# Optimization experiments

Hardware: AMD Instinct MI355X
Metric: run time of the kernel (lower is better)

Reference implementation:

```python
import jax, jax.numpy as jnp
import numpy as np

N_NODES = 100000
N_EDGES = 1600000
IN_F = 128
HEADS = 4
D_K = 32
OUT_TOTAL = HEADS * D_K


def setup_inputs() -> dict:
    key = jax.random.key(0)
    k1, k2, k3, k4, k5, k6 = jax.random.split(key, 6)
    x = jax.random.normal(k1, (N_NODES, IN_F), dtype=jnp.float32)
    edge_index = jax.random.randint(k2, (2, N_EDGES), 0, N_NODES, dtype=jnp.int64)
    # torch nn.Linear weights: [out, in], xavier-uniform init
    def xavier(k, shape):
        fan_out, fan_in = shape
        lim = float(np.sqrt(6.0 / (fan_in + fan_out)))
        return jax.random.uniform(k, shape, dtype=jnp.float32, minval=-lim, maxval=lim)
    Wq = xavier(k3, (OUT_TOTAL, IN_F))
    Wk = xavier(k4, (OUT_TOTAL, IN_F))
    Wv = xavier(k5, (OUT_TOTAL, IN_F))
    # D init_type='uniform': U(-1, 1)
    D = jax.random.uniform(k6, (HEADS, D_K), dtype=jnp.float32, minval=-1.0, maxval=1.0)
    return {"x": x, "Wq": Wq, "Wk": Wk, "Wv": Wv, "D": D, "edge_index": edge_index}


def reference(x, Wq, Wk, Wv, D, edge_index):
    N = x.shape[0]
    scale = 1.0 / np.sqrt(D_K)
    Q = (x @ Wq.T).reshape(N, HEADS, D_K)
    K = (x @ Wk.T).reshape(N, HEADS, D_K)
    V = (x @ Wv.T).reshape(N, HEADS, D_K)
    row, col = edge_index[0], edge_index[1]
    K_i = K[row]              # [E, H, d]
    Q_j = Q[col]              # [E, H, d]
    diff = K_i - Q_j
    # non-self edges: diff^T diag(D) diff ; self edges: K^T diag(D) Q
    score_edge = jnp.sum(diff * D * diff, axis=-1)          # [E, H]
    score_self = jnp.sum(K_i * D * Q[row], axis=-1)         # [E, H]
    self_mask = (row == col)[:, None]
    scores = jnp.where(self_mask, score_self, score_edge)
    scores = jax.nn.leaky_relu(scores * scale, 0.2)
    # segment softmax over destination node `row`
    smax = jax.ops.segment_max(scores, row, num_segments=N)  # [N, H]
    ex = jnp.exp(scores - smax[row])
    ssum = jax.ops.segment_sum(ex, row, num_segments=N)      # [N, H]
    alpha = ex / (ssum[row] + 1e-16)
    # scatter-add aggregate alpha * V[col] into destination rows
    out = jax.ops.segment_sum(alpha[:, :, None] * V[col], row, num_segments=N)
    return out.reshape(N, OUT_TOTAL)
```

## Files before the change

kernel.cpp:

```cpp
#include <hip/hip_runtime.h>
#include <hip/hip_fp16.h>
#include <cmath>


#define HEADS 4
#define DK 32
#define FDIM 128
#define BINSHIFT 8
#define BINCAP 6144

typedef _Float16 f16x8 __attribute__((ext_vector_type(8)));
typedef float f32x4 __attribute__((ext_vector_type(4)));

__global__ __launch_bounds__(256) void split_w(
    const float* __restrict__ Wq, const float* __restrict__ Wk,
    const float* __restrict__ Wv, _Float16* __restrict__ Whf,
    _Float16* __restrict__ Wlf, int* __restrict__ bin_cursor, int nb)
{
    const int gid = blockIdx.x * 256 + threadIdx.x;
    if (gid < nb) bin_cursor[gid] = 0;

    const int p = blockIdx.x;
    const float* __restrict__ W = (p == 0) ? Wq : (p == 1 ? Wk : Wv);
#pragma unroll
    for (int i = 0; i < 8; ++i) {
        const int id = i * 256 + threadIdx.x;
        const int g  = id >> 8;
        const int kc = (id >> 6) & 3;
        const int l  = id & 63;
        const int row  = g * 16 + (l & 15);
        const int col0 = kc * 32 + (l >> 4) * 8;
        const float* src = W + row * FDIM + col0;
        const float4 v0 = *reinterpret_cast<const float4*>(src);
        const float4 v1 = *reinterpret_cast<const float4*>(src + 4);
        const float vv[8] = {v0.x, v0.y, v0.z, v0.w, v1.x, v1.y, v1.z, v1.w};
        f16x8 h, lo;
#pragma unroll
        for (int j = 0; j < 8; ++j) {
            _Float16 hh = (_Float16)vv[j];
            h[j]  = hh;
            lo[j] = (_Float16)(vv[j] - (float)hh);
        }
        const size_t off = ((size_t)((p * 8 + g) * 4 + kc) * 64 + l) * 8;
        *reinterpret_cast<f16x8*>(Whf + off) = h;
        *reinterpret_cast<f16x8*>(Wlf + off) = lo;
    }
}

__device__ __forceinline__ int swz_idx(int row, int kk) {
    return (row * FDIM + kk) ^ ((row & 7) << 3);
}

__device__ __forceinline__ void stage_x(
    const float* __restrict__ src, _Float16* __restrict__ dh,
    _Float16* __restrict__ dl, int n0, int nmax, int tid)
{
    const int kk0 = (tid & 15) * 8;
    const int r0  = tid >> 4;
#pragma unroll
    for (int i = 0; i < 4; ++i) {
        const int row = i * 16 + r0;
        float4 v0 = make_float4(0.f, 0.f, 0.f, 0.f), v1 = v0;
        if (n0 + row < nmax) {
            const float* p = src + (size_t)(n0 + row) * FDIM + kk0;
            v0 = *reinterpret_cast<const float4*>(p);
            v1 = *reinterpret_cast<const float4*>(p + 4);
        }
        const float vv[8] = {v0.x, v0.y, v0.z, v0.w, v1.x, v1.y, v1.z, v1.w};
        f16x8 h, l;
#pragma unroll
        for (int j = 0; j < 8; ++j) {
            _Float16 hh = (_Float16)vv[j];
            h[j] = hh;
            l[j] = (_Float16)(vv[j] - (float)hh);
        }
        const int si = swz_idx(row, kk0);
        *reinterpret_cast<f16x8*>(&dh[si]) = h;
        *reinterpret_cast<f16x8*>(&dl[si]) = l;
    }
}

__global__ __launch_bounds__(256) void qkv_and_partition(
    const float* __restrict__ x, const _Float16* __restrict__ Whf,
    const _Float16* __restrict__ Wlf, __half* __restrict__ QVh,
    float* __restrict__ Kout, int N, int NQ, int NF,
    const int* __restrict__ row, const int* __restrict__ col,
    int* __restrict__ bin_cursor, unsigned* __restrict__ pairs, int E, int NB)
{
    __shared__ __align__(16) char smem[32768];

    const long T = (long)NQ + NF;
    const long bid = blockIdx.x;
    const int fprev = (int)((bid * NF) / T);
    const int fcur  = (int)(((bid + 1) * NF) / T);

    if (fcur > fprev) {
        int* hist  = (int*)smem;
        int* basea = hist + 512;
        int* cura  = basea + 512;
        const int tid = threadIdx.x;
        for (int b = tid; b < 512; b += 256) { hist[b] = 0; cura[b] = 0; }
        __syncthreads();

        const int e0 = fprev * 4096;
        int rr[16], cc[16];
        if (e0 + 4096 <= E) {
#pragma unroll
            for (int i = 0; i < 4; ++i) {
                const int idx = e0 + i * 1024 + tid * 4;
                const int4 r4 = *reinterpret_cast<const int4*>(row + idx);
                const int4 c4 = *reinterpret_cast<const int4*>(col + idx);
                rr[i*4+0] = r4.x; rr[i*4+1] = r4.y; rr[i*4+2] = r4.z; rr[i*4+3] = r4.w;
                cc[i*4+0] = c4.x; cc[i*4+1] = c4.y; cc[i*4+2] = c4.z; cc[i*4+3] = c4.w;
            }
        } else {
#pragma unroll
            for (int i = 0; i < 4; ++i)
#pragma unroll
                for (int j = 0; j < 4; ++j) {
                    const int idx = e0 + i * 1024 + tid * 4 + j;
                    rr[i*4+j] = (idx < E) ? row[idx] : -1;
                    cc[i*4+j] = (idx < E) ? col[idx] : 0;
                }
        }

#pragma unroll
        for (int i = 0; i < 16; ++i)
            if ((unsigned)rr[i] < (unsigned)N)
                atomicAdd(&hist[rr[i] >> BINSHIFT], 1);
        __syncthreads();

        for (int b = tid; b < NB; b += 256) {
            const int h = hist[b];
            basea[b] = h ? atomicAdd(&bin_cursor[b], h) : 0;
        }
        __syncthreads();

#pragma unroll
        for (int i = 0; i < 16; ++i) {
            const int r = rr[i];
            if ((unsigned)r < (unsigned)N) {
                const int b = r >> BINSHIFT;
                const int p = basea[b] + atomicAdd(&cura[b], 1);
                if (p < BINCAP)
                    pairs[(size_t)b * BINCAP + p] =
                        (unsigned)(r & 255) | ((unsigned)cc[i] << 8);
            }
        }
        return;
    }

    _Float16* xh = (_Float16*)smem;
    _Float16* xl = (_Float16*)(smem + 16384);

    const int qidx = (int)bid - fprev;
    const int n0  = qidx * 64;
    const int tid = threadIdx.x;
    const int lane = tid & 63;
    const int wv   = tid >> 6;
    const int wr0  = (wv >> 1) * 32;
    const int wc0  = (wv & 1) * 64;
    const int g0   = wc0 >> 4;
    const int orow = (lane >> 4) * 4;
    const int ocol = lane & 15;

    stage_x(x, xh, xl, n0, N, tid);
    __syncthreads();

    const int lrow = lane & 15;
    const int lk   = (lane >> 4) * 8;

    for (int p = 0; p < 3; ++p) {
        f32x4 acc[2][4];
#pragma unroll
        for (int a = 0; a < 2; ++a)
#pragma unroll
            for (int b = 0; b < 4; ++b)
                acc[a][b] = (f32x4){0.f, 0.f, 0.f, 0.f};

#pragma unroll
        for (int kc = 0; kc < 4; ++kc) {
            f16x8 afh[2], afl[2], bfh[4], bfl[4];
#pragma unroll
            for (int a = 0; a < 2; ++a) {
                const int si = swz_idx(wr0 + a * 16 + lrow, kc * 32 + lk);
                afh[a] = *reinterpret_cast<const f16x8*>(&xh[si]);
                afl[a] = *reinterpret_cast<const f16x8*>(&xl[si]);
            }
#pragma unroll
            for (int b = 0; b < 4; ++b) {
                const size_t off =
                    ((size_t)((p * 8 + g0 + b) * 4 + kc) * 64 + lane) * 8;
                bfh[b] = *reinterpret_cast<const f16x8*>(Whf + off);
                bfl[b] = *reinterpret_cast<const f16x8*>(Wlf + off);
            }
#pragma unroll
            for (int a = 0; a < 2; ++a)
#pragma unroll
                for (int b = 0; b < 4; ++b)
                    acc[a][b] = __builtin_amdgcn_mfma_f32_16x16x32_f16(
                        afh[a], bfh[b], acc[a][b], 0, 0, 0);
#pragma unroll
            for (int a = 0; a < 2; ++a)
#pragma unroll
                for (int b = 0; b < 4; ++b)
                    acc[a][b] = __builtin_amdgcn_mfma_f32_16x16x32_f16(
                        afl[a], bfh[b], acc[a][b], 0, 0, 0);
#pragma unroll
            for (int a = 0; a < 2; ++a)
#pragma unroll
                for (int b = 0; b < 4; ++b)
                    acc[a][b] = __builtin_amdgcn_mfma_f32_16x16x32_f16(
                        afh[a], bfl[b], acc[a][b], 0, 0, 0);
        }

        if (p == 1) {
#pragma unroll
            for (int a = 0; a < 2; ++a) {
#pragma unroll
                for (int r = 0; r < 4; ++r) {
                    const int n = n0 + wr0 + a * 16 + orow + r;
                    if (n < N) {
                        float* op = Kout + (size_t)n * FDIM + wc0 + ocol;
#pragma unroll
                        for (int b = 0; b < 4; ++b)
                            op[b * 16] = acc[a][b][r];
                    }
                }
            }
        } else {
            const int voff = (p == 2) ? 4 : 0;
#pragma unroll
            for (int a = 0; a < 2; ++a) {
#pragma unroll
                for (int r = 0; r < 4; ++r) {
                    const int n = n0 + wr0 + a * 16 + orow + r;
                    if (n < N) {
                        __half* op = QVh + (size_t)n * 256;
#pragma unroll
                        for (int b = 0; b < 4; ++b) {
                            const int d_o = wc0 + ocol + b * 16;
                            op[((d_o >> 2) << 3) + (d_o & 3) + voff] =
                                __float2half(acc[a][b][r]);
                        }
                    }
                }
            }
        }
    }
}

__global__ __launch_bounds__(256) void build_csr(
    const int* __restrict__ bin_cursor, const unsigned* __restrict__ pairs,
    int* __restrict__ csr, int* __restrict__ offA, int* __restrict__ cntA,
    int N)
{
    __shared__ int deg[256];
    __shared__ int offs[256];
    __shared__ int cur[256];
    const int b = blockIdx.x;
    const int tid = threadIdx.x;
    deg[tid] = 0;
    __syncthreads();

    int nsize = bin_cursor[b];
    if (nsize > BINCAP) nsize = BINCAP;
    const unsigned* bp = pairs + (size_t)b * BINCAP;

    for (int i = tid; i < nsize; i += 256)
        atomicAdd(&deg[bp[i] & 255], 1);
    __syncthreads();

    const int v = deg[tid];
    offs[tid] = v;
    __syncthreads();
    for (int o = 1; o < 256; o <<= 1) {
        const int t = (tid >= o) ? offs[tid - o] : 0;
        __syncthreads();
        offs[tid] += t;
        __syncthreads();
    }
    const int excl = offs[tid] - v;
    cur[tid] = excl;
    const int node = (b << BINSHIFT) + tid;
    if (node < N) {
        offA[node] = b * BINCAP + excl;
        cntA[node] = v;
    }
    __syncthreads();

    for (int i = tid; i < nsize; i += 256) {
        const unsigned pv = bp[i];
        const int p = atomicAdd(&cur[pv & 255], 1);
        csr[(size_t)b * BINCAP + p] = (int)((pv >> 8) << 9);
    }
}

__global__ __launch_bounds__(256) void fused_aggregate(
    const int* __restrict__ offA, const int* __restrict__ cntA,
    const int* __restrict__ csr, const __half* __restrict__ QVh,
    const float* Kb, const float* __restrict__ D, float* out, int N)
{
    int node = blockIdx.x * 4 + (threadIdx.x >> 6);
    if (node >= N) return;
    const int lane = threadIdx.x & 63;
    const int hl   = lane & 31;
    const int side = lane >> 5;
    const int d0   = hl << 2;
    const float4 kv = *reinterpret_cast<const float4*>(Kb + (size_t)node * FDIM + d0);
    const float4 Dv = *reinterpret_cast<const float4*>(D + d0);
    const float Dk0 = Dv.x * kv.x, Dk1 = Dv.y * kv.y,
                Dk2 = Dv.z * kv.z, Dk3 = Dv.w * kv.w;
    const int j0  = offA[node];
    const int cnt = cntA[node];
    const int nb  = node << 9;
    float a0 = 0.f, a1 = 0.f, a2 = 0.f, a3 = 0.f, se = 0.f;

    int cc0, cc1, cc2, cc3;
    float4 t0, t1, t2, t3;

#define LOADP(s, p) { int c_ = __shfl(ecb, 2 * (p) + side); cc##s = c_; \
    t##s = *reinterpret_cast<const float4*>( \
        reinterpret_cast<const char*>(QVh) + (size_t)(unsigned)c_ + (hl << 4)); }

#define PROCP(s) { \
    const __half2* th = reinterpret_cast<const __half2*>(&t##s); \
    float2 q01 = __half22float2(th[0]); float2 q23 = __half22float2(th[1]); \
    float2 v01 = __half22float2(th[2]); float2 v23 = __half22float2(th[3]); \
    float p; \
    if (cc##s == nb) { \
        p = Dk0 * q01.x + Dk1 * q01.y + Dk2 * q23.x + Dk3 * q23.y; \
    } else { \
        float e0 = kv.x - q01.x, e1 = kv.y - q01.y; \
        float e2 = kv.z - q23.x, e3 = kv.w - q23.y; \
        p = Dv.x*e0*e0 + Dv.y*e1*e1 + Dv.z*e2*e2 + Dv.w*e3*e3; \
    } \
    p += __shfl_xor(p, 1); p += __shfl_xor(p, 2); p += __shfl_xor(p, 4); \
    float z = p * 0.17677669529663687f; \
    z = fmaxf(z, 0.2f * z); \
    float ex = __expf(z); \
    a0 += ex * v01.x; a1 += ex * v01.y; \
    a2 += ex * v23.x; a3 += ex * v23.y; se += ex; }

    for (int base = 0; base < cnt; base += 64) {
        const int rem = min(64, cnt - base);
        const int ecb = (lane < rem) ? csr[j0 + base + lane] : 0;
        const int npair = rem >> 1;
        int pj = 0;
        if (npair >= 4) {
            LOADP(0, 0) LOADP(1, 1) LOADP(2, 2) LOADP(3, 3)
            while (pj + 8 <= npair) {
                PROCP(0) LOADP(0, pj + 4)
                PROCP(1) LOADP(1, pj + 5)
                PROCP(2) LOADP(2, pj + 6)
                PROCP(3) LOADP(3, pj + 7)
                pj += 4;
            }
            PROCP(0) PROCP(1) PROCP(2) PROCP(3)
            pj += 4;
        }
        for (; pj < npair; ++pj) {
            LOADP(0, pj)
            PROCP(0)
        }
        if (rem & 1) {
            const int c_ = __shfl(ecb, rem - 1);
            float4 tt = *reinterpret_cast<const float4*>(
                reinterpret_cast<const char*>(QVh) + (size_t)(unsigned)c_ + (hl << 4));
            const __half2* th = reinterpret_cast<const __half2*>(&tt);
            float2 q01 = __half22float2(th[0]); float2 q23 = __half22float2(th[1]);
            float2 v01 = __half22float2(th[2]); float2 v23 = __half22float2(th[3]);
            float p;
            if (c_ == nb) {
                p = Dk0 * q01.x + Dk1 * q01.y + Dk2 * q23.x + Dk3 * q23.y;
            } else {
                float e0 = kv.x - q01.x, e1 = kv.y - q01.y;
                float e2 = kv.z - q23.x, e3 = kv.w - q23.y;
                p = Dv.x*e0*e0 + Dv.y*e1*e1 + Dv.z*e2*e2 + Dv.w*e3*e3;
            }
            p += __shfl_xor(p, 1); p += __shfl_xor(p, 2); p += __shfl_xor(p, 4);
            float z = p * 0.17677669529663687f;
            z = fmaxf(z, 0.2f * z);
            float ex = __expf(z) * 0.5f;
            a0 += ex * v01.x; a1 += ex * v01.y;
            a2 += ex * v23.x; a3 += ex * v23.y; se += ex;
        }
    }
#undef LOADP
#undef PROCP

    a0 += __shfl_xor(a0, 32); a1 += __shfl_xor(a1, 32);
    a2 += __shfl_xor(a2, 32); a3 += __shfl_xor(a3, 32);
    se += __shfl_xor(se, 32);

    if (side == 0) {
        const float inv = 1.0f / (se + 1e-16f);
        *reinterpret_cast<float4*>(out + (size_t)node * FDIM + d0) =
            make_float4(a0 * inv, a1 * inv, a2 * inv, a3 * inv);
    }
}

extern "C" void kernel_launch(void* const* d_in, const int* in_sizes, int n_in,
                              void* d_out, int out_size, void* d_ws, size_t ws_size,
                              hipStream_t stream) {
    const float* x  = (const float*)d_in[0];
    const float* Wq = (const float*)d_in[1];
    const float* Wk = (const float*)d_in[2];
    const float* Wv = (const float*)d_in[3];
    const float* D  = (const float*)d_in[4];
    const int*  edge = (const int*)d_in[5];
    float* out = (float*)d_out;

    const int N = in_sizes[0] / FDIM;
    const int E = in_sizes[5] / 2;
    const int* row = edge;
    const int* col = edge + E;

    const int NB = (N + 255) >> 8;

    __half* QVh = (__half*)d_ws;
    unsigned* pairs = (unsigned*)(QVh + (size_t)N * 256);
    int* csr  = (int*)(pairs + (size_t)NB * BINCAP);
    int* offA = csr + (size_t)NB * BINCAP;
    int* cntA = offA + N;
    int* bin_cursor = cntA + N;
    _Float16* Whf = (_Float16*)(bin_cursor + 512);
    _Float16* Wlf = Whf + 3 * 16384;
    float* Kout = out;

    const int NQ = (N + 63) / 64;
    const int NF = (E + 4095) / 4096;

    split_w<<<3, 256, 0, stream>>>(Wq, Wk, Wv, Whf, Wlf, bin_cursor, NB);

    qkv_and_partition<<<NQ + NF, 256, 0, stream>>>(
        x, Whf, Wlf, QVh, Kout, N, NQ, NF, row, col, bin_cursor, pairs, E, NB);

    build_csr<<<NB, 256, 0, stream>>>(
        bin_cursor, pairs, csr, offA, cntA, N);

    fused_aggregate<<<(N + 3) / 4, 256, 0, stream>>>(
        offA, cntA, csr, QVh, Kout, D, out, N);
}
```

Baseline: 296.4 us.

## Regroup kernel stages: partition with weight split, CSR build with QKV GEMM

The edge partition moves out of the QKV kernel and into a first kernel that also converts the weights to split fp16. The per-bin CSR build moves into the QKV GEMM kernel, so it overlaps with the projection work instead of running as its own launch. The bin cursor is now zeroed with a memset, which keeps the kernel count at four but removes one serial stage. The partition no longer overlaps with the GEMM and now runs in its own short kernel before it.

```diff
diff --git a/kernel.cpp b/kernel.cpp
--- a/kernel.cpp
+++ b/kernel.cpp
@@ -12,38 +12,95 @@
 typedef _Float16 f16x8 __attribute__((ext_vector_type(8)));
 typedef float f32x4 __attribute__((ext_vector_type(4)));
 
-__global__ __launch_bounds__(256) void split_w(
+__global__ __launch_bounds__(256) void partition_and_splitw(
+    const int* __restrict__ row, const int* __restrict__ col,
+    int* __restrict__ bin_cursor, unsigned* __restrict__ pairs,
+    int E, int N, int NB, int NF,
     const float* __restrict__ Wq, const float* __restrict__ Wk,
     const float* __restrict__ Wv, _Float16* __restrict__ Whf,
-    _Float16* __restrict__ Wlf, int* __restrict__ bin_cursor, int nb)
+    _Float16* __restrict__ Wlf)
 {
-    const int gid = blockIdx.x * 256 + threadIdx.x;
-    if (gid < nb) bin_cursor[gid] = 0;
-
-    const int p = blockIdx.x;
-    const float* __restrict__ W = (p == 0) ? Wq : (p == 1 ? Wk : Wv);
-#pragma unroll
-    for (int i = 0; i < 8; ++i) {
-        const int id = i * 256 + threadIdx.x;
-        const int g  = id >> 8;
-        const int kc = (id >> 6) & 3;
-        const int l  = id & 63;
-        const int row  = g * 16 + (l & 15);
-        const int col0 = kc * 32 + (l >> 4) * 8;
-        const float* src = W + row * FDIM + col0;
-        const float4 v0 = *reinterpret_cast<const float4*>(src);
-        const float4 v1 = *reinterpret_cast<const float4*>(src + 4);
-        const float vv[8] = {v0.x, v0.y, v0.z, v0.w, v1.x, v1.y, v1.z, v1.w};
-        f16x8 h, lo;
-#pragma unroll
-        for (int j = 0; j < 8; ++j) {
-            _Float16 hh = (_Float16)vv[j];
-            h[j]  = hh;
-            lo[j] = (_Float16)(vv[j] - (float)hh);
-        }
-        const size_t off = ((size_t)((p * 8 + g) * 4 + kc) * 64 + l) * 8;
-        *reinterpret_cast<f16x8*>(Whf + off) = h;
-        *reinterpret_cast<f16x8*>(Wlf + off) = lo;
+    __shared__ int hist[512];
+    __shared__ int basea[512];
+    __shared__ int cura[512];
+    const int tid = threadIdx.x;
+
+    if ((int)blockIdx.x >= NF) {
+        const int p = blockIdx.x - NF;
+        const float* __restrict__ W = (p == 0) ? Wq : (p == 1 ? Wk : Wv);
+#pragma unroll
+        for (int i = 0; i < 8; ++i) {
+            const int id = i * 256 + tid;
+            const int g  = id >> 8;
+            const int kc = (id >> 6) & 3;
+            const int l  = id & 63;
+            const int rw   = g * 16 + (l & 15);
+            const int col0 = kc * 32 + (l >> 4) * 8;
+            const float* src = W + rw * FDIM + col0;
+            const float4 v0 = *reinterpret_cast<const float4*>(src);
+            const float4 v1 = *reinterpret_cast<const float4*>(src + 4);
+            const float vv[8] = {v0.x, v0.y, v0.z, v0.w, v1.x, v1.y, v1.z, v1.w};
+            f16x8 h, lo;
+#pragma unroll
+            for (int j = 0; j < 8; ++j) {
+                _Float16 hh = (_Float16)vv[j];
+                h[j]  = hh;
+                lo[j] = (_Float16)(vv[j] - (float)hh);
+            }
+            const size_t off = ((size_t)((p * 8 + g) * 4 + kc) * 64 + l) * 8;
+            *reinterpret_cast<f16x8*>(Whf + off) = h;
+            *reinterpret_cast<f16x8*>(Wlf + off) = lo;
+        }
+        return;
+    }
+
+    for (int b = tid; b < 512; b += 256) { hist[b] = 0; cura[b] = 0; }
+    __syncthreads();
+
+    const int e0 = blockIdx.x * 4096;
+    int rr[16], cc[16];
+    if (e0 + 4096 <= E) {
+#pragma unroll
+        for (int i = 0; i < 4; ++i) {
+            const int idx = e0 + i * 1024 + tid * 4;
+            const int4 r4 = *reinterpret_cast<const int4*>(row + idx);
+            const int4 c4 = *reinterpret_cast<const int4*>(col + idx);
+            rr[i*4+0] = r4.x; rr[i*4+1] = r4.y; rr[i*4+2] = r4.z; rr[i*4+3] = r4.w;
+            cc[i*4+0] = c4.x; cc[i*4+1] = c4.y; cc[i*4+2] = c4.z; cc[i*4+3] = c4.w;
+        }
+    } else {
+#pragma unroll
+        for (int i = 0; i < 4; ++i)
+#pragma unroll
+            for (int j = 0; j < 4; ++j) {
+                const int idx = e0 + i * 1024 + tid * 4 + j;
+                rr[i*4+j] = (idx < E) ? row[idx] : -1;
+                cc[i*4+j] = (idx < E) ? col[idx] : 0;
+            }
+    }
+
+#pragma unroll
+    for (int i = 0; i < 16; ++i)
+        if ((unsigned)rr[i] < (unsigned)N)
+            atomicAdd(&hist[rr[i] >> BINSHIFT], 1);
+    __syncthreads();
+
+    for (int b = tid; b < NB; b += 256) {
+        const int h = hist[b];
+        basea[b] = h ? atomicAdd(&bin_cursor[b], h) : 0;
+    }
+    __syncthreads();
+
+#pragma unroll
+    for (int i = 0; i < 16; ++i) {
+        const int r = rr[i];
+        if ((unsigned)r < (unsigned)N) {
+            const int b = r >> BINSHIFT;
+            const int p = basea[b] + atomicAdd(&cura[b], 1);
+            if (p < BINCAP)
+                pairs[(size_t)b * BINCAP + p] =
+                    (unsigned)(r & 255) | ((unsigned)cc[i] << 8);
+        }
     }
 }
 
@@ -80,72 +137,59 @@
     }
 }
 
-__global__ __launch_bounds__(256) void qkv_and_partition(
+__global__ __launch_bounds__(256) void qkv_and_build(
     const float* __restrict__ x, const _Float16* __restrict__ Whf,
     const _Float16* __restrict__ Wlf, __half* __restrict__ QVh,
-    float* __restrict__ Kout, int N, int NQ, int NF,
-    const int* __restrict__ row, const int* __restrict__ col,
-    int* __restrict__ bin_cursor, unsigned* __restrict__ pairs, int E, int NB)
+    float* __restrict__ Kout, int N, int NQ, int NB,
+    const int* __restrict__ bin_cursor, const unsigned* __restrict__ pairs,
+    int* __restrict__ csr, int* __restrict__ offA, int* __restrict__ cntA)
 {
     __shared__ __align__(16) char smem[32768];
 
-    const long T = (long)NQ + NF;
+    const long T = (long)NQ + NB;
     const long bid = blockIdx.x;
-    const int fprev = (int)((bid * NF) / T);
-    const int fcur  = (int)(((bid + 1) * NF) / T);
+    const int fprev = (int)((bid * NB) / T);
+    const int fcur  = (int)(((bid + 1) * NB) / T);
 
     if (fcur > fprev) {
-        int* hist  = (int*)smem;
-        int* basea = hist + 512;
-        int* cura  = basea + 512;
+        int* deg  = (int*)smem;
+        int* offs = deg + 256;
+        int* cur  = offs + 256;
+        const int b = fprev;
         const int tid = threadIdx.x;
-        for (int b = tid; b < 512; b += 256) { hist[b] = 0; cura[b] = 0; }
+        deg[tid] = 0;
         __syncthreads();
 
-        const int e0 = fprev * 4096;
-        int rr[16], cc[16];
-        if (e0 + 4096 <= E) {
-#pragma unroll
-            for (int i = 0; i < 4; ++i) {
-                const int idx = e0 + i * 1024 + tid * 4;
-                const int4 r4 = *reinterpret_cast<const int4*>(row + idx);
-                const int4 c4 = *reinterpret_cast<const int4*>(col + idx);
-                rr[i*4+0] = r4.x; rr[i*4+1] = r4.y; rr[i*4+2] = r4.z; rr[i*4+3] = r4.w;
-                cc[i*4+0] = c4.x; cc[i*4+1] = c4.y; cc[i*4+2] = c4.z; cc[i*4+3] = c4.w;
-            }
-        } else {
-#pragma unroll
-            for (int i = 0; i < 4; ++i)
-#pragma unroll
-                for (int j = 0; j < 4; ++j) {
-                    const int idx = e0 + i * 1024 + tid * 4 + j;
-                    rr[i*4+j] = (idx < E) ? row[idx] : -1;
-                    cc[i*4+j] = (idx < E) ? col[idx] : 0;
-                }
-        }
-
-#pragma unroll
-        for (int i = 0; i < 16; ++i)
-            if ((unsigned)rr[i] < (unsigned)N)
-                atomicAdd(&hist[rr[i] >> BINSHIFT], 1);
+        int nsize = bin_cursor[b];
+        if (nsize > BINCAP) nsize = BINCAP;
+        const unsigned* bp = pairs + (size_t)b * BINCAP;
+
+        for (int i = tid; i < nsize; i += 256)
+            atomicAdd(&deg[bp[i] & 255], 1);
         __syncthreads();
 
-        for (int b = tid; b < NB; b += 256) {
-            const int h = hist[b];
-            basea[b] = h ? atomicAdd(&bin_cursor[b], h) : 0;
-        }
+        const int v = deg[tid];
+        offs[tid] = v;
         __syncthreads();
-
-#pragma unroll
-        for (int i = 0; i < 16; ++i) {
-            const int r = rr[i];
-            if ((unsigned)r < (unsigned)N) {
-                const int b = r >> BINSHIFT;
-                const int p = basea[b] + atomicAdd(&cura[b], 1);
-                if (p < BINCAP)
-                    pairs[(size_t)b * BINCAP + p] =
-                        (unsigned)(r & 255) | ((unsigned)cc[i] << 8);
-            }
+        for (int o = 1; o < 256; o <<= 1) {
+            const int t = (tid >= o) ? offs[tid - o] : 0;
+            __syncthreads();
+            offs[tid] += t;
+            __syncthreads();
+        }
+        const int excl = offs[tid] - v;
+        cur[tid] = excl;
+        const int node = (b << BINSHIFT) + tid;
+        if (node < N) {
+            offA[node] = b * BINCAP + excl;
+            cntA[node] = v;
+        }
+        __syncthreads();
+
+        for (int i = tid; i < nsize; i += 256) {
+            const unsigned pv = bp[i];
+            const int p = atomicAdd(&cur[pv & 255], 1);
+            csr[(size_t)b * BINCAP + p] = (int)((pv >> 8) << 9);
         }
         return;
     }
@@ -247,52 +291,6 @@
                 }
             }
         }
-    }
-}
-
-__global__ __launch_bounds__(256) void build_csr(
-    const int* __restrict__ bin_cursor, const unsigned* __restrict__ pairs,
-    int* __restrict__ csr, int* __restrict__ offA, int* __restrict__ cntA,
-    int N)
-{
-    __shared__ int deg[256];
-    __shared__ int offs[256];
-    __shared__ int cur[256];
-    const int b = blockIdx.x;
-    const int tid = threadIdx.x;
-    deg[tid] = 0;
-    __syncthreads();
-
-    int nsize = bin_cursor[b];
-    if (nsize > BINCAP) nsize = BINCAP;
-    const unsigned* bp = pairs + (size_t)b * BINCAP;
-
-    for (int i = tid; i < nsize; i += 256)
-        atomicAdd(&deg[bp[i] & 255], 1);
-    __syncthreads();
-
-    const int v = deg[tid];
-    offs[tid] = v;
-    __syncthreads();
-    for (int o = 1; o < 256; o <<= 1) {
-        const int t = (tid >= o) ? offs[tid - o] : 0;
-        __syncthreads();
-        offs[tid] += t;
-        __syncthreads();
-    }
-    const int excl = offs[tid] - v;
-    cur[tid] = excl;
-    const int node = (b << BINSHIFT) + tid;
-    if (node < N) {
-        offA[node] = b * BINCAP + excl;
-        cntA[node] = v;
-    }
-    __syncthreads();
-
-    for (int i = tid; i < nsize; i += 256) {
-        const unsigned pv = bp[i];
-        const int p = atomicAdd(&cur[pv & 255], 1);
-        csr[(size_t)b * BINCAP + p] = (int)((pv >> 8) << 9);
     }
 }
 
@@ -431,13 +429,13 @@
     const int NQ = (N + 63) / 64;
     const int NF = (E + 4095) / 4096;
 
-    split_w<<<3, 256, 0, stream>>>(Wq, Wk, Wv, Whf, Wlf, bin_cursor, NB);
-
-    qkv_and_partition<<<NQ + NF, 256, 0, stream>>>(
-        x, Whf, Wlf, QVh, Kout, N, NQ, NF, row, col, bin_cursor, pairs, E, NB);
-
-    build_csr<<<NB, 256, 0, stream>>>(
-        bin_cursor, pairs, csr, offA, cntA, N);
+    hipMemsetAsync(bin_cursor, 0, (size_t)NB * sizeof(int), stream);
+
+    partition_and_splitw<<<NF + 3, 256, 0, stream>>>(
+        row, col, bin_cursor, pairs, E, N, NB, NF, Wq, Wk, Wv, Whf, Wlf);
+
+    qkv_and_build<<<NQ + NB, 256, 0, stream>>>(
+        x, Whf, Wlf, QVh, Kout, N, NQ, NB, bin_cursor, pairs, csr, offA, cntA);
 
     fused_aggregate<<<(N + 3) / 4, 256, 0, stream>>>(
         offA, cntA, csr, QVh, Kout, D, out, N);
```

New measurement: 299.8 us. Within noise of the previous version (+1.1%).
